# Kernel optimization log

Hardware: AMD Instinct MI355X
Metric: run time of the kernel (lower is better)

Reference implementation:

```python
import jax, jax.numpy as jnp
import numpy as np

N, D, E = 100000, 128, 800000

def setup_inputs() -> dict:
    key = jax.random.key(0)
    k1, k2, k3, k4 = jax.random.split(key, 4)
    z = jax.random.normal(k1, (N, D), dtype=jnp.float32)
    edge_index = jax.random.randint(k2, (2, E), 0, N, dtype=jnp.int64)
    # PyTorch-style init scale for Linear layers (kaiming-uniform-ish via normal is fine for a numeric reference)
    W1 = jax.random.normal(k3, (2 * D, D), dtype=jnp.float32) * (1.0 / np.sqrt(2 * D))
    b1 = jnp.zeros((D,), dtype=jnp.float32)
    W2 = jax.random.normal(k4, (D, 1), dtype=jnp.float32) * (1.0 / np.sqrt(D))
    b2 = jnp.zeros((1,), dtype=jnp.float32)
    return {"z": z, "edge_index": edge_index, "W1": W1, "b1": b1, "W2": W2, "b2": b2}

def reference(z, edge_index, W1, b1, W2, b2):
    # row/col gather of node embeddings
    row, col = edge_index[0], edge_index[1]
    # cat([z[row], z[col]]) @ W1 == z[row] @ W1[:D] + z[col] @ W1[D:]
    # -> avoids materializing the [E, 2D] concatenated tensor
    d = z.shape[1]
    h = z[row] @ W1[:d] + z[col] @ W1[d:] + b1          # [E, D]
    h = jax.nn.relu(h)                                   # Dropout(0.1) is identity in eval mode
    out = h @ W2 + b2                                    # [E, 1]
    return out.squeeze(-1)                               # [E]
```

## Files before the change

### kernel.cpp

```cpp
#include <hip/hip_runtime.h>

#define DDIM 128

typedef __bf16 bf16x8 __attribute__((ext_vector_type(8)));
typedef float  floatx4 __attribute__((ext_vector_type(4)));

__device__ inline unsigned short f2bf(float f) {
    unsigned u = __builtin_bit_cast(unsigned, f);
    u += 0x7fffu + ((u >> 16) & 1u);
    return (unsigned short)(u >> 16);
}

#define EPI_B 136

__global__ __launch_bounds__(256) void precompute_uv_mfma_q8(
    const float* __restrict__ z, const float* __restrict__ W1,
    const float* __restrict__ b1,
    signed char* __restrict__ U8, signed char* __restrict__ V8,
    float* __restrict__ u_scale, float* __restrict__ v_scale,
    int N, int nchunks)
{
    __shared__ unsigned short WsF[32 * 64 * 8];
    __shared__ __attribute__((aligned(16))) unsigned char epi[64 * EPI_B];

    const int t    = threadIdx.x;
    const int lane = t & 63;
    const int w    = t >> 6;
    const int half = blockIdx.x;
    signed char* __restrict__ dst8 = half ? V8 : U8;
    float*       __restrict__ dscl = half ? v_scale : u_scale;
    const float* __restrict__ Wh   = W1 + (size_t)half * DDIM * DDIM;

    {
        const int nlow = lane & 15;
        const int kq   = (lane >> 4) & 3;
        #pragma unroll
        for (int i = 0; i < 8; ++i) {
            const int ntks = w + i * 4;
            const int nt = ntks >> 2, ks = ntks & 3;
            const int n  = nt * 16 + nlow;
            const int kb = ks * 32 + kq * 8;
            unsigned short frag[8];
            #pragma unroll
            for (int j = 0; j < 8; ++j)
                frag[j] = f2bf(Wh[(kb + j) * DDIM + n]);
            *(uint4*)&WsF[(ntks * 64 + lane) * 8] = *(const uint4*)frag;
        }
    }
    __syncthreads();

    const int mrow = lane & 15;
    const int quad = lane >> 4;

    float bval[8];
    #pragma unroll
    for (int nt = 0; nt < 8; ++nt)
        bval[nt] = (half == 0) ? b1[nt * 16 + mrow] : 0.f;

    for (int chunk = blockIdx.y; chunk < nchunks; chunk += gridDim.y) {
        const int m0 = chunk * 64 + w * 16;

        bf16x8 afrag[4];
        {
            int grow = m0 + mrow; if (grow > N - 1) grow = N - 1;
            const float* zrow = z + (size_t)grow * DDIM;
            #pragma unroll
            for (int ks = 0; ks < 4; ++ks) {
                const int k0 = ks * 32 + quad * 8;
                const float4 x0 = *(const float4*)(zrow + k0);
                const float4 x1 = *(const float4*)(zrow + k0 + 4);
                unsigned short a[8];
                a[0] = f2bf(x0.x); a[1] = f2bf(x0.y); a[2] = f2bf(x0.z); a[3] = f2bf(x0.w);
                a[4] = f2bf(x1.x); a[5] = f2bf(x1.y); a[6] = f2bf(x1.z); a[7] = f2bf(x1.w);
                afrag[ks] = __builtin_bit_cast(bf16x8, *(const uint4*)a);
            }
        }

        floatx4 acc[8];
        #pragma unroll
        for (int nt = 0; nt < 8; ++nt) acc[nt] = (floatx4){0.f, 0.f, 0.f, 0.f};

        #pragma unroll
        for (int ks = 0; ks < 4; ++ks) {
            #pragma unroll
            for (int nt = 0; nt < 8; ++nt) {
                const bf16x8 b = __builtin_bit_cast(bf16x8,
                    *(const uint4*)&WsF[((nt * 4 + ks) * 64 + lane) * 8]);
                acc[nt] = __builtin_amdgcn_mfma_f32_16x16x32_bf16(afrag[ks], b, acc[nt], 0, 0, 0);
            }
        }

        #pragma unroll
        for (int r = 0; r < 4; ++r) {
            float mx = 0.f;
            #pragma unroll
            for (int nt = 0; nt < 8; ++nt)
                mx = fmaxf(mx, fabsf(acc[nt][r] + bval[nt]));
            #pragma unroll
            for (int m = 1; m < 16; m <<= 1)
                mx = fmaxf(mx, __shfl_xor(mx, m, 16));
            mx = fmaxf(mx, 1e-20f);
            const float inv = 127.f / mx;

            unsigned char bytes[8];
            #pragma unroll
            for (int nt = 0; nt < 8; ++nt) {
                const float v = (acc[nt][r] + bval[nt]) * inv;
                const int q = (int)rintf(v);
                bytes[nt] = (unsigned char)(q & 0xff);
            }
            const int lrow = w * 16 + quad * 4 + r;
            *(unsigned long long*)&epi[lrow * EPI_B + mrow * 8] =
                *(const unsigned long long*)bytes;

            if (mrow == 0) {
                const int grow = chunk * 64 + lrow;
                if (grow < N) dscl[grow] = mx * (1.f / 127.f);
            }
        }
        __builtin_amdgcn_s_waitcnt(0);

        {
            const int cg = lane & 15;
            const int r2 = lane >> 4;
            #pragma unroll
            for (int it = 0; it < 4; ++it) {
                const int lr   = it * 4 + r2;
                const int lrow = w * 16 + lr;
                const uint2 dat = *(const uint2*)&epi[lrow * EPI_B + cg * 8];
                const int grow = chunk * 64 + lrow;
                if (grow < N)
                    *(uint2*)&dst8[(size_t)grow * DDIM + cg * 8] = dat;
            }
        }
    }
}

__global__ __launch_bounds__(256) void edge_kernel_i8(
    const int* __restrict__ ei,
    const signed char* __restrict__ U8, const signed char* __restrict__ V8,
    const float* __restrict__ u_scale, const float* __restrict__ v_scale,
    const float* __restrict__ W2, const float* __restrict__ b2,
    float* __restrict__ out, int E)
{
    const int t  = threadIdx.x;
    const int p  = t & 15;
    const int g0 = (blockIdx.x * 16 + (t >> 4)) * 4;

    float ww[8];
    #pragma unroll
    for (int j = 0; j < 8; ++j) ww[j] = W2[j * 16 + p];

    if (g0 >= E) return;

    int rows[4], cols[4];
    if (g0 + 3 < E) {
        const int4 r4 = *(const int4*)(ei + g0);
        const int4 c4 = *(const int4*)(ei + (size_t)E + g0);
        rows[0]=r4.x; rows[1]=r4.y; rows[2]=r4.z; rows[3]=r4.w;
        cols[0]=c4.x; cols[1]=c4.y; cols[2]=c4.z; cols[3]=c4.w;
    } else {
        #pragma unroll
        for (int i = 0; i < 4; ++i) {
            const int gi = (g0 + i < E) ? (g0 + i) : (E - 1);
            rows[i] = ei[gi];
            cols[i] = ei[(size_t)E + gi];
        }
    }

    uint2 uu[4], vv[4];
    #pragma unroll
    for (int i = 0; i < 4; ++i)
        uu[i] = *(const uint2*)(U8 + (size_t)rows[i] * DDIM + p * 8);
    #pragma unroll
    for (int i = 0; i < 4; ++i)
        vv[i] = *(const uint2*)(V8 + (size_t)cols[i] * DDIM + p * 8);

    float su[4], sv[4];
    #pragma unroll
    for (int i = 0; i < 4; ++i) { su[i] = u_scale[rows[i]]; sv[i] = v_scale[cols[i]]; }

    const float bias = b2[0];

    #pragma unroll
    for (int i = 0; i < 4; ++i) {
        const signed char* us = (const signed char*)&uu[i];
        const signed char* vs = (const signed char*)&vv[i];
        float s = 0.f;
        #pragma unroll
        for (int j = 0; j < 8; ++j) {
            const float h = fmaf(sv[i], (float)vs[j], su[i] * (float)us[j]);
            s = fmaf(fmaxf(h, 0.f), ww[j], s);
        }
        #pragma unroll
        for (int off = 8; off > 0; off >>= 1)
            s += __shfl_down(s, off, 16);
        if (p == 0 && g0 + i < E) out[g0 + i] = s + bias;
    }
}

__global__ __launch_bounds__(256) void edge_fused_fallback(
    const float* __restrict__ z, const int* __restrict__ ei,
    const float* __restrict__ W1, const float* __restrict__ b1,
    const float* __restrict__ W2, const float* __restrict__ b2,
    float* __restrict__ out, int N, int E)
{
    const int tid  = blockIdx.x * 256 + threadIdx.x;
    const int e    = tid >> 6;
    const int lane = tid & 63;
    if (e >= E) return;

    const int row = ei[e];
    const int col = ei[(size_t)E + e];
    const float* zr = z + (size_t)row * DDIM;
    const float* zc = z + (size_t)col * DDIM;

    float h0 = b1[lane];
    float h1 = b1[lane + 64];
    for (int k = 0; k < DDIM; ++k) {
        const float a = zr[k];
        const float b = zc[k];
        h0 = fmaf(a, W1[k * DDIM + lane],               h0);
        h0 = fmaf(b, W1[(DDIM + k) * DDIM + lane],      h0);
        h1 = fmaf(a, W1[k * DDIM + lane + 64],          h1);
        h1 = fmaf(b, W1[(DDIM + k) * DDIM + lane + 64], h1);
    }
    float s = fmaxf(h0, 0.f) * W2[lane] + fmaxf(h1, 0.f) * W2[lane + 64];
    #pragma unroll
    for (int off = 32; off > 0; off >>= 1)
        s += __shfl_down(s, off, 64);
    if (lane == 0) out[e] = s + b2[0];
}

extern "C" void kernel_launch(void* const* d_in, const int* in_sizes, int n_in,
                              void* d_out, int out_size, void* d_ws, size_t ws_size,
                              hipStream_t stream)
{
    const float* z  = (const float*)d_in[0];
    const int*   ei = (const int*)d_in[1];
    const float* W1 = (const float*)d_in[2];
    const float* b1 = (const float*)d_in[3];
    const float* W2 = (const float*)d_in[4];
    const float* b2 = (const float*)d_in[5];
    float*       out = (float*)d_out;

    const int N = in_sizes[0] / DDIM;
    const int E = in_sizes[1] / 2;

    const size_t n128 = (size_t)N * DDIM;
    const size_t need = 2 * n128 + 2 * (size_t)N * sizeof(float) + 256;
    if (ws_size >= need) {
        signed char* U8 = (signed char*)d_ws;
        signed char* V8 = U8 + n128;
        float* usc = (float*)(((size_t)(V8 + n128) + 255) & ~(size_t)255);
        float* vsc = usc + N;
        const int nchunks = (N + 63) / 64;
        hipLaunchKernelGGL(precompute_uv_mfma_q8, dim3(2, 384), dim3(256), 0, stream,
                           z, W1, b1, U8, V8, usc, vsc, N, nchunks);
        hipLaunchKernelGGL(edge_kernel_i8, dim3((E + 63) / 64), dim3(256), 0, stream,
                           ei, U8, V8, usc, vsc, W2, b2, out, E);
    } else {
        hipLaunchKernelGGL(edge_fused_fallback, dim3((E + 3) / 4), dim3(256), 0, stream,
                           z, ei, W1, b1, W2, b2, out, N, E);
    }
}
```

Measured before the change: 140.8 us.

## Fuse U and V projections into one pass over z with direct stores

The precompute kernel now computes both halves of the first linear layer in one block, loading the full W1 into LDS and running 16 MFMA N-tiles per chunk. The separate launch dimension per half is removed. z is read and converted to bf16 once instead of twice. The LDS-staged epilogue is replaced with direct 8-byte global stores per lane. In exchange, register pressure and LDS use double, which may lower occupancy.

```diff
diff --git a/kernel.cpp b/kernel.cpp
--- a/kernel.cpp
+++ b/kernel.cpp
@@ -10,8 +10,6 @@
     u += 0x7fffu + ((u >> 16) & 1u);
     return (unsigned short)(u >> 16);
 }
-
-#define EPI_B 136
 
 __global__ __launch_bounds__(256) void precompute_uv_mfma_q8(
     const float* __restrict__ z, const float* __restrict__ W1,
@@ -20,30 +18,28 @@
     float* __restrict__ u_scale, float* __restrict__ v_scale,
     int N, int nchunks)
 {
-    __shared__ unsigned short WsF[32 * 64 * 8];
-    __shared__ __attribute__((aligned(16))) unsigned char epi[64 * EPI_B];
+    __shared__ unsigned short WsF[64 * 64 * 8];
 
     const int t    = threadIdx.x;
     const int lane = t & 63;
     const int w    = t >> 6;
-    const int half = blockIdx.x;
-    signed char* __restrict__ dst8 = half ? V8 : U8;
-    float*       __restrict__ dscl = half ? v_scale : u_scale;
-    const float* __restrict__ Wh   = W1 + (size_t)half * DDIM * DDIM;
 
     {
         const int nlow = lane & 15;
         const int kq   = (lane >> 4) & 3;
         #pragma unroll
-        for (int i = 0; i < 8; ++i) {
+        for (int i = 0; i < 16; ++i) {
             const int ntks = w + i * 4;
             const int nt = ntks >> 2, ks = ntks & 3;
             const int n  = nt * 16 + nlow;
             const int kb = ks * 32 + kq * 8;
+            const float* __restrict__ wsrc = (n < DDIM)
+                ? (W1 + (size_t)kb * DDIM + n)
+                : (W1 + (size_t)(DDIM + kb) * DDIM + (n - DDIM));
             unsigned short frag[8];
             #pragma unroll
             for (int j = 0; j < 8; ++j)
-                frag[j] = f2bf(Wh[(kb + j) * DDIM + n]);
+                frag[j] = f2bf(wsrc[(size_t)j * DDIM]);
             *(uint4*)&WsF[(ntks * 64 + lane) * 8] = *(const uint4*)frag;
         }
     }
@@ -52,12 +48,12 @@
     const int mrow = lane & 15;
     const int quad = lane >> 4;
 
-    float bval[8];
-    #pragma unroll
-    for (int nt = 0; nt < 8; ++nt)
-        bval[nt] = (half == 0) ? b1[nt * 16 + mrow] : 0.f;
-
-    for (int chunk = blockIdx.y; chunk < nchunks; chunk += gridDim.y) {
+    float bval[16];
+    #pragma unroll
+    for (int nt = 0; nt < 16; ++nt)
+        bval[nt] = (nt < 8) ? b1[nt * 16 + mrow] : 0.f;
+
+    for (int chunk = blockIdx.x; chunk < nchunks; chunk += gridDim.x) {
         const int m0 = chunk * 64 + w * 16;
 
         bf16x8 afrag[4];
@@ -76,14 +72,14 @@
             }
         }
 
-        floatx4 acc[8];
-        #pragma unroll
-        for (int nt = 0; nt < 8; ++nt) acc[nt] = (floatx4){0.f, 0.f, 0.f, 0.f};
+        floatx4 acc[16];
+        #pragma unroll
+        for (int nt = 0; nt < 16; ++nt) acc[nt] = (floatx4){0.f, 0.f, 0.f, 0.f};
 
         #pragma unroll
         for (int ks = 0; ks < 4; ++ks) {
             #pragma unroll
-            for (int nt = 0; nt < 8; ++nt) {
+            for (int nt = 0; nt < 16; ++nt) {
                 const bf16x8 b = __builtin_bit_cast(bf16x8,
                     *(const uint4*)&WsF[((nt * 4 + ks) * 64 + lane) * 8]);
                 acc[nt] = __builtin_amdgcn_mfma_f32_16x16x32_bf16(afrag[ks], b, acc[nt], 0, 0, 0);
@@ -92,45 +88,38 @@
 
         #pragma unroll
         for (int r = 0; r < 4; ++r) {
-            float mx = 0.f;
-            #pragma unroll
-            for (int nt = 0; nt < 8; ++nt)
-                mx = fmaxf(mx, fabsf(acc[nt][r] + bval[nt]));
-            #pragma unroll
-            for (int m = 1; m < 16; m <<= 1)
-                mx = fmaxf(mx, __shfl_xor(mx, m, 16));
-            mx = fmaxf(mx, 1e-20f);
-            const float inv = 127.f / mx;
-
-            unsigned char bytes[8];
+            float au = 0.f, av = 0.f;
+            #pragma unroll
+            for (int nt = 0; nt < 8; ++nt)  au = fmaxf(au, fabsf(acc[nt][r] + bval[nt]));
+            #pragma unroll
+            for (int nt = 8; nt < 16; ++nt) av = fmaxf(av, fabsf(acc[nt][r]));
+            #pragma unroll
+            for (int m = 1; m < 16; m <<= 1) {
+                au = fmaxf(au, __shfl_xor(au, m, 16));
+                av = fmaxf(av, __shfl_xor(av, m, 16));
+            }
+            au = fmaxf(au, 1e-20f); av = fmaxf(av, 1e-20f);
+            const float iu = 127.f / au, iv = 127.f / av;
+
+            unsigned char bu[8], bv[8];
             #pragma unroll
             for (int nt = 0; nt < 8; ++nt) {
-                const float v = (acc[nt][r] + bval[nt]) * inv;
-                const int q = (int)rintf(v);
-                bytes[nt] = (unsigned char)(q & 0xff);
-            }
-            const int lrow = w * 16 + quad * 4 + r;
-            *(unsigned long long*)&epi[lrow * EPI_B + mrow * 8] =
-                *(const unsigned long long*)bytes;
-
-            if (mrow == 0) {
-                const int grow = chunk * 64 + lrow;
-                if (grow < N) dscl[grow] = mx * (1.f / 127.f);
-            }
-        }
-        __builtin_amdgcn_s_waitcnt(0);
-
-        {
-            const int cg = lane & 15;
-            const int r2 = lane >> 4;
-            #pragma unroll
-            for (int it = 0; it < 4; ++it) {
-                const int lr   = it * 4 + r2;
-                const int lrow = w * 16 + lr;
-                const uint2 dat = *(const uint2*)&epi[lrow * EPI_B + cg * 8];
-                const int grow = chunk * 64 + lrow;
-                if (grow < N)
-                    *(uint2*)&dst8[(size_t)grow * DDIM + cg * 8] = dat;
+                const int qu = (int)rintf((acc[nt][r] + bval[nt]) * iu);
+                const int qv = (int)rintf(acc[nt + 8][r] * iv);
+                bu[nt] = (unsigned char)(qu & 0xff);
+                bv[nt] = (unsigned char)(qv & 0xff);
+            }
+
+            const int grow = chunk * 64 + w * 16 + quad * 4 + r;
+            if (grow < N) {
+                *(unsigned long long*)&U8[(size_t)grow * DDIM + mrow * 8] =
+                    *(const unsigned long long*)bu;
+                *(unsigned long long*)&V8[(size_t)grow * DDIM + mrow * 8] =
+                    *(const unsigned long long*)bv;
+                if (mrow == 0) {
+                    u_scale[grow] = au * (1.f / 127.f);
+                    v_scale[grow] = av * (1.f / 127.f);
+                }
             }
         }
     }
@@ -255,7 +244,7 @@
         float* usc = (float*)(((size_t)(V8 + n128) + 255) & ~(size_t)255);
         float* vsc = usc + N;
         const int nchunks = (N + 63) / 64;
-        hipLaunchKernelGGL(precompute_uv_mfma_q8, dim3(2, 384), dim3(256), 0, stream,
+        hipLaunchKernelGGL(precompute_uv_mfma_q8, dim3(512), dim3(256), 0, stream,
                            z, W1, b1, U8, V8, usc, vsc, N, nchunks);
         hipLaunchKernelGGL(edge_kernel_i8, dim3((E + 63) / 64), dim3(256), 0, stream,
                            ei, U8, V8, usc, vsc, W2, b2, out, E);
```

New measurement: 153.4 us. 1.09x slower.

## Pre-swizzle W1 into bf16 fragments once and compute U and V per block

Applied to the files above, without the earlier changes.

Adds a small kernel that converts W1 to bf16 MFMA fragment layout in workspace once per call. The precompute kernel then reads B fragments straight from global memory (L2-cached) rather than rebuilding them in LDS in each block. Each block now handles both halves (U and V) for one 64-row chunk, so z is loaded and converted only once, with one block per chunk instead of a persistent grid. It also drops the LDS epilogue staging in favor of direct 8-byte stores. The trade-offs are an extra kernel launch, more uncoalesced stores, and global-memory fragment loads replacing LDS reads.

```diff
diff --git a/kernel.cpp b/kernel.cpp
--- a/kernel.cpp
+++ b/kernel.cpp
@@ -11,81 +11,77 @@
     return (unsigned short)(u >> 16);
 }
 
-#define EPI_B 136
-
-__global__ __launch_bounds__(256) void precompute_uv_mfma_q8(
-    const float* __restrict__ z, const float* __restrict__ W1,
+__global__ __launch_bounds__(256) void swizzle_w(
+    const float* __restrict__ W1, unsigned short* __restrict__ Wf)
+{
+    const int id   = blockIdx.x * 256 + threadIdx.x;
+    const int f    = id >> 6;
+    const int lane = id & 63;
+    const int nt = f >> 2, ks = f & 3;
+    const int n  = nt * 16 + (lane & 15);
+    const int kb = ks * 32 + (lane >> 4) * 8;
+    const float* __restrict__ wsrc = (n < DDIM)
+        ? (W1 + (size_t)kb * DDIM + n)
+        : (W1 + (size_t)(DDIM + kb) * DDIM + (n - DDIM));
+    unsigned short frag[8];
+    #pragma unroll
+    for (int j = 0; j < 8; ++j)
+        frag[j] = f2bf(wsrc[(size_t)j * DDIM]);
+    *(uint4*)&Wf[(size_t)id * 8] = *(const uint4*)frag;
+}
+
+__global__ __launch_bounds__(256, 3) void precompute_uv_mfma_q8(
+    const float* __restrict__ z, const unsigned short* __restrict__ Wf,
     const float* __restrict__ b1,
     signed char* __restrict__ U8, signed char* __restrict__ V8,
     float* __restrict__ u_scale, float* __restrict__ v_scale,
-    int N, int nchunks)
-{
-    __shared__ unsigned short WsF[32 * 64 * 8];
-    __shared__ __attribute__((aligned(16))) unsigned char epi[64 * EPI_B];
-
-    const int t    = threadIdx.x;
-    const int lane = t & 63;
-    const int w    = t >> 6;
-    const int half = blockIdx.x;
-    signed char* __restrict__ dst8 = half ? V8 : U8;
-    float*       __restrict__ dscl = half ? v_scale : u_scale;
-    const float* __restrict__ Wh   = W1 + (size_t)half * DDIM * DDIM;
-
-    {
-        const int nlow = lane & 15;
-        const int kq   = (lane >> 4) & 3;
-        #pragma unroll
-        for (int i = 0; i < 8; ++i) {
-            const int ntks = w + i * 4;
-            const int nt = ntks >> 2, ks = ntks & 3;
-            const int n  = nt * 16 + nlow;
-            const int kb = ks * 32 + kq * 8;
-            unsigned short frag[8];
-            #pragma unroll
-            for (int j = 0; j < 8; ++j)
-                frag[j] = f2bf(Wh[(kb + j) * DDIM + n]);
-            *(uint4*)&WsF[(ntks * 64 + lane) * 8] = *(const uint4*)frag;
-        }
-    }
-    __syncthreads();
-
+    int N)
+{
+    const int lane = threadIdx.x & 63;
+    const int w    = threadIdx.x >> 6;
     const int mrow = lane & 15;
     const int quad = lane >> 4;
-
-    float bval[8];
-    #pragma unroll
-    for (int nt = 0; nt < 8; ++nt)
-        bval[nt] = (half == 0) ? b1[nt * 16 + mrow] : 0.f;
-
-    for (int chunk = blockIdx.y; chunk < nchunks; chunk += gridDim.y) {
-        const int m0 = chunk * 64 + w * 16;
-
-        bf16x8 afrag[4];
-        {
-            int grow = m0 + mrow; if (grow > N - 1) grow = N - 1;
-            const float* zrow = z + (size_t)grow * DDIM;
-            #pragma unroll
-            for (int ks = 0; ks < 4; ++ks) {
-                const int k0 = ks * 32 + quad * 8;
-                const float4 x0 = *(const float4*)(zrow + k0);
-                const float4 x1 = *(const float4*)(zrow + k0 + 4);
-                unsigned short a[8];
-                a[0] = f2bf(x0.x); a[1] = f2bf(x0.y); a[2] = f2bf(x0.z); a[3] = f2bf(x0.w);
-                a[4] = f2bf(x1.x); a[5] = f2bf(x1.y); a[6] = f2bf(x1.z); a[7] = f2bf(x1.w);
-                afrag[ks] = __builtin_bit_cast(bf16x8, *(const uint4*)a);
-            }
-        }
+    const int m0   = blockIdx.x * 64 + w * 16;
+
+    bf16x8 afrag[4];
+    {
+        int grow = m0 + mrow; if (grow > N - 1) grow = N - 1;
+        const float* zrow = z + (size_t)grow * DDIM;
+        #pragma unroll
+        for (int ks = 0; ks < 4; ++ks) {
+            const int k0 = ks * 32 + quad * 8;
+            const float4 x0 = *(const float4*)(zrow + k0);
+            const float4 x1 = *(const float4*)(zrow + k0 + 4);
+            unsigned short a[8];
+            a[0] = f2bf(x0.x); a[1] = f2bf(x0.y); a[2] = f2bf(x0.z); a[3] = f2bf(x0.w);
+            a[4] = f2bf(x1.x); a[5] = f2bf(x1.y); a[6] = f2bf(x1.z); a[7] = f2bf(x1.w);
+            afrag[ks] = __builtin_bit_cast(bf16x8, *(const uint4*)a);
+        }
+    }
+
+    #pragma unroll
+    for (int half = 0; half < 2; ++half) {
+        signed char* __restrict__ dst8 = half ? V8 : U8;
+        float*       __restrict__ dscl = half ? v_scale : u_scale;
+
+        float bval[8];
+        #pragma unroll
+        for (int nt = 0; nt < 8; ++nt)
+            bval[nt] = half ? 0.f : b1[nt * 16 + mrow];
 
         floatx4 acc[8];
         #pragma unroll
         for (int nt = 0; nt < 8; ++nt) acc[nt] = (floatx4){0.f, 0.f, 0.f, 0.f};
+
+        const unsigned short* __restrict__ wbase =
+            Wf + ((size_t)half * 32 * 64) * 8 + (size_t)lane * 8;
 
         #pragma unroll
         for (int ks = 0; ks < 4; ++ks) {
             #pragma unroll
             for (int nt = 0; nt < 8; ++nt) {
                 const bf16x8 b = __builtin_bit_cast(bf16x8,
-                    *(const uint4*)&WsF[((nt * 4 + ks) * 64 + lane) * 8]);
+                    *(const uint4*)(wbase + (size_t)((nt * 4 + ks) * 64) * 8));
                 acc[nt] = __builtin_amdgcn_mfma_f32_16x16x32_bf16(afrag[ks], b, acc[nt], 0, 0, 0);
             }
         }
@@ -105,32 +101,14 @@
             unsigned char bytes[8];
             #pragma unroll
             for (int nt = 0; nt < 8; ++nt) {
-                const float v = (acc[nt][r] + bval[nt]) * inv;
-                const int q = (int)rintf(v);
+                const int q = (int)rintf((acc[nt][r] + bval[nt]) * inv);
                 bytes[nt] = (unsigned char)(q & 0xff);
             }
-            const int lrow = w * 16 + quad * 4 + r;
-            *(unsigned long long*)&epi[lrow * EPI_B + mrow * 8] =
-                *(const unsigned long long*)bytes;
-
-            if (mrow == 0) {
-                const int grow = chunk * 64 + lrow;
-                if (grow < N) dscl[grow] = mx * (1.f / 127.f);
-            }
-        }
-        __builtin_amdgcn_s_waitcnt(0);
-
-        {
-            const int cg = lane & 15;
-            const int r2 = lane >> 4;
-            #pragma unroll
-            for (int it = 0; it < 4; ++it) {
-                const int lr   = it * 4 + r2;
-                const int lrow = w * 16 + lr;
-                const uint2 dat = *(const uint2*)&epi[lrow * EPI_B + cg * 8];
-                const int grow = chunk * 64 + lrow;
-                if (grow < N)
-                    *(uint2*)&dst8[(size_t)grow * DDIM + cg * 8] = dat;
+            const int grow = m0 + quad * 4 + r;
+            if (grow < N) {
+                *(unsigned long long*)&dst8[(size_t)grow * DDIM + mrow * 8] =
+                    *(const unsigned long long*)bytes;
+                if (mrow == 0) dscl[grow] = mx * (1.f / 127.f);
             }
         }
     }
@@ -248,15 +226,18 @@
     const int E = in_sizes[1] / 2;
 
     const size_t n128 = (size_t)N * DDIM;
-    const size_t need = 2 * n128 + 2 * (size_t)N * sizeof(float) + 256;
+    const size_t need = 2 * n128 + 2 * (size_t)N * sizeof(float)
+                      + 64 * 1024 + 512;
     if (ws_size >= need) {
         signed char* U8 = (signed char*)d_ws;
         signed char* V8 = U8 + n128;
         float* usc = (float*)(((size_t)(V8 + n128) + 255) & ~(size_t)255);
         float* vsc = usc + N;
-        const int nchunks = (N + 63) / 64;
-        hipLaunchKernelGGL(precompute_uv_mfma_q8, dim3(2, 384), dim3(256), 0, stream,
-                           z, W1, b1, U8, V8, usc, vsc, N, nchunks);
+        unsigned short* Wf = (unsigned short*)(((size_t)(vsc + N) + 255) & ~(size_t)255);
+
+        hipLaunchKernelGGL(swizzle_w, dim3(16), dim3(256), 0, stream, W1, Wf);
+        hipLaunchKernelGGL(precompute_uv_mfma_q8, dim3((N + 63) / 64), dim3(256), 0, stream,
+                           z, Wf, b1, U8, V8, usc, vsc, N);
         hipLaunchKernelGGL(edge_kernel_i8, dim3((E + 63) / 64), dim3(256), 0, stream,
                            ei, U8, V8, usc, vsc, W2, b2, out, E);
     } else {
```

Result: slower. 146.7 us (+4.2%).
